# Kernel optimization log

Measured on AMD Instinct MI355X. Metric: run time of the kernel, lower is better.

Reference implementation:

```python
import jax, jax.numpy as jnp
import numpy as np

BIT = 8
QMAX = 2 ** (BIT - 1) - 1          # 127
QMIN = -(2 ** (BIT - 1))           # -128
BOUNDARY_RANGE = 0.005
EPS = 1e-5


def _quant_act_int8(x):
    # StatsQ per-tensor activation quantization: scale from (1 - boundary_range)
    # quantile of |x| (robust absmax), fake-quant with STE.
    amax = jnp.maximum(jnp.quantile(jnp.abs(x), 1.0 - BOUNDARY_RANGE), EPS)
    s = QMAX / amax
    q = jnp.clip(jnp.round(x * s), QMIN, QMAX) / s
    return x + jax.lax.stop_gradient(q - x)


def _quant_w_ternary(w):
    # BitNet-1.58-style per-tensor ternary weight quantization:
    # gamma = mean(|W|); W_q in {-1, 0, +1} * gamma; STE.
    gamma = jnp.mean(jnp.abs(w)) + EPS
    q = jnp.clip(jnp.round(w / gamma), -1.0, 1.0) * gamma
    return w + jax.lax.stop_gradient(q - w)


def _qlinear(x, w):
    # quantize activations (int8 fake-quant) and weights (ternary), then matmul
    xq = _quant_act_int8(x)
    wq = _quant_w_ternary(w)
    return jnp.einsum('btd,hd->bth', xq, wq)


def _layernorm(x, g, b):
    mu = jnp.mean(x, axis=-1, keepdims=True)
    var = jnp.mean(jnp.square(x - mu), axis=-1, keepdims=True)
    return (x - mu) * jax.lax.rsqrt(var + 1e-5) * g + b


def setup_inputs() -> dict:
    key = jax.random.key(0)
    k_x, k_w1, k_w2 = jax.random.split(key, 3)
    B, T, D, H = 64, 256, 1024, 4096
    x = jax.random.normal(k_x, (B, T, D), dtype=jnp.float32)
    ln_g = jnp.ones((D,), dtype=jnp.float32)
    ln_b = jnp.zeros((D,), dtype=jnp.float32)
    w1 = jax.random.normal(k_w1, (H, D), dtype=jnp.float32) * (1.0 / np.sqrt(D))
    w2 = jax.random.normal(k_w2, (D, H), dtype=jnp.float32) * (1.0 / np.sqrt(H))
    return {'x': x, 'ln_g': ln_g, 'ln_b': ln_b, 'w1': w1, 'w2': w2}


def reference(x, ln_g, ln_b, w1, w2):
    h = _layernorm(x, ln_g, ln_b)          # [B,T,D]
    h = _qlinear(h, w1)                    # [B,T,H]
    h = jax.nn.gelu(h, approximate=False)  # torch nn.GELU default = exact erf
    out = _qlinear(h, w2)                  # [B,T,D]
    return out
```

## Files before the change

kernel.cpp:

```cpp
#include <hip/hip_runtime.h>
#include <hip/hip_fp16.h>
#include <math.h>


#define M_ROWS 16384
#define D_DIM  1024
#define H_DIM  4096

typedef int i32x4 __attribute__((ext_vector_type(4)));

#define AS1 __attribute__((address_space(1)))
#define AS3 __attribute__((address_space(3)))

__device__ __forceinline__ void load_lds16(const void* g, void* l) {
  __builtin_amdgcn_global_load_lds((const AS1 void*)g, (AS3 void*)l, 16, 0, 0);
}

__device__ __forceinline__ float block_sum256(float v, float* lds) {
#pragma unroll
  for (int o = 32; o > 0; o >>= 1) v += __shfl_down(v, o, 64);
  int t = threadIdx.x;
  __syncthreads();
  if ((t & 63) == 0) lds[t >> 6] = v;
  __syncthreads();
  return lds[0] + lds[1] + lds[2] + lds[3];
}

__global__ __launch_bounds__(256) void k_layernorm(
    const float* __restrict__ x, const float* __restrict__ g,
    const float* __restrict__ b, __half* __restrict__ out) {
  __shared__ float lds[4];
  int row = blockIdx.x, t = threadIdx.x;
  float4 v = ((const float4*)(x + (size_t)row * D_DIM))[t];
  float s = v.x + v.y + v.z + v.w;
  s = block_sum256(s, lds);
  float mu = s * (1.0f / D_DIM);
  float d0 = v.x - mu, d1 = v.y - mu, d2 = v.z - mu, d3 = v.w - mu;
  float ss = d0 * d0 + d1 * d1 + d2 * d2 + d3 * d3;
  ss = block_sum256(ss, lds);
  float inv = 1.0f / sqrtf(ss * (1.0f / D_DIM) + 1e-5f);
  float4 gg = ((const float4*)g)[t];
  float4 bb = ((const float4*)b)[t];
  __half2 p0 = __floats2half2_rn(d0 * inv * gg.x + bb.x, d1 * inv * gg.y + bb.y);
  __half2 p1 = __floats2half2_rn(d2 * inv * gg.z + bb.z, d3 * inv * gg.w + bb.w);
  uint2 st;
  st.x = *(unsigned*)&p0;
  st.y = *(unsigned*)&p1;
  ((uint2*)(out + (size_t)row * D_DIM))[t] = st;
}

__global__ __launch_bounds__(256) void k_absmean(const float4* __restrict__ p,
                                                 size_t n4, double* __restrict__ out) {
  double s = 0.0;
  size_t stride = (size_t)gridDim.x * blockDim.x;
  for (size_t i = (size_t)blockIdx.x * blockDim.x + threadIdx.x; i < n4; i += stride) {
    float4 v = p[i];
    s += (double)fabsf(v.x) + (double)fabsf(v.y) + (double)fabsf(v.z) + (double)fabsf(v.w);
  }
#pragma unroll
  for (int o = 32; o > 0; o >>= 1) s += __shfl_down(s, o, 64);
  __shared__ double ds[4];
  int t = threadIdx.x;
  if ((t & 63) == 0) ds[t >> 6] = s;
  __syncthreads();
  if (t == 0) atomicAdd(out, ds[0] + ds[1] + ds[2] + ds[3]);
}

__device__ __forceinline__ int tern1(float w, float gamma) {
  return (int)fminf(1.f, fmaxf(-1.f, rintf(w / gamma)));
}

__global__ __launch_bounds__(256) void k_wquant(const float4* __restrict__ w,
                                                unsigned* __restrict__ wq, size_t n4,
                                                const double* __restrict__ sump,
                                                double inv_n, float* __restrict__ gamma_out) {
  float gamma = (float)(*sump * inv_n) + 1e-5f;
  if (blockIdx.x == 0 && threadIdx.x == 0) *gamma_out = gamma;
  size_t stride = (size_t)gridDim.x * blockDim.x;
  for (size_t i = (size_t)blockIdx.x * blockDim.x + threadIdx.x; i < n4; i += stride) {
    float4 v = w[i];
    int a = tern1(v.x, gamma), b = tern1(v.y, gamma), c = tern1(v.z, gamma), d = tern1(v.w, gamma);
    wq[i] = (unsigned)(a & 255) | ((unsigned)(b & 255) << 8) |
            ((unsigned)(c & 255) << 16) | ((unsigned)(d & 255) << 24);
  }
}

__global__ __launch_bounds__(512) void k_hist16(const uint4* __restrict__ p, size_t n8,
                                                unsigned* __restrict__ hist) {
  extern __shared__ unsigned h[];
  int t = threadIdx.x;
  for (int i = t; i < 32768; i += 512) h[i] = 0;
  __syncthreads();
  size_t stride = (size_t)gridDim.x * 512;
  for (size_t i = (size_t)blockIdx.x * 512 + t; i < n8; i += stride) {
    uint4 u = p[i];
    atomicAdd(&h[u.x & 0x7FFFu], 1u);
    atomicAdd(&h[(u.x >> 16) & 0x7FFFu], 1u);
    atomicAdd(&h[u.y & 0x7FFFu], 1u);
    atomicAdd(&h[(u.y >> 16) & 0x7FFFu], 1u);
    atomicAdd(&h[u.z & 0x7FFFu], 1u);
    atomicAdd(&h[(u.z >> 16) & 0x7FFFu], 1u);
    atomicAdd(&h[u.w & 0x7FFFu], 1u);
    atomicAdd(&h[(u.w >> 16) & 0x7FFFu], 1u);
  }
  __syncthreads();
  for (int i = t; i < 32768; i += 512) {
    unsigned c = h[i];
    if (c) atomicAdd(&hist[i], c);
  }
}

__global__ __launch_bounds__(256) void k_scanq(const unsigned* __restrict__ hist,
                                               float* __restrict__ scl,
                                               unsigned long long k, double frac) {
  __shared__ unsigned tsum[256];
  __shared__ unsigned long long pre[256];
  __shared__ unsigned vk, vk1;
  int t = threadIdx.x;
  unsigned s = 0;
  for (int j = 0; j < 128; ++j) s += hist[t * 128 + j];
  tsum[t] = s;
  __syncthreads();
  if (t == 0) {
    unsigned long long c = 0;
    for (int i = 0; i < 256; ++i) { pre[i] = c; c += tsum[i]; }
  }
  __syncthreads();
  unsigned long long base = pre[t];
  for (int j = 0; j < 128; ++j) {
    unsigned c = hist[t * 128 + j];
    if (base <= k && k < base + c) vk = t * 128 + j;
    if (base <= k + 1 && k + 1 < base + c) vk1 = t * 128 + j;
    base += c;
  }
  __syncthreads();
  if (t == 0) {
    double a = (double)__half2float(__ushort_as_half((unsigned short)vk));
    double b = (double)__half2float(__ushort_as_half((unsigned short)vk1));
    double qv = (frac >= 0.5) ? (b - (b - a) * (1.0 - frac)) : (a + (b - a) * frac);
    float amax = fmaxf((float)qv, 1e-5f);
    scl[0] = amax;
    scl[1] = 127.0f / amax;
  }
}

__device__ __forceinline__ void unpack8(uint4 u, float* f) {
  __half2 h;
  h = *(__half2*)&u.x; f[0] = __low2float(h); f[1] = __high2float(h);
  h = *(__half2*)&u.y; f[2] = __low2float(h); f[3] = __high2float(h);
  h = *(__half2*)&u.z; f[4] = __low2float(h); f[5] = __high2float(h);
  h = *(__half2*)&u.w; f[6] = __low2float(h); f[7] = __high2float(h);
}

__device__ __forceinline__ unsigned qpack4(float a, float b, float c, float d, float s) {
  int qa = (int)fminf(127.f, fmaxf(-128.f, rintf(a * s)));
  int qb = (int)fminf(127.f, fmaxf(-128.f, rintf(b * s)));
  int qc = (int)fminf(127.f, fmaxf(-128.f, rintf(c * s)));
  int qd = (int)fminf(127.f, fmaxf(-128.f, rintf(d * s)));
  return (unsigned)(qa & 255) | ((unsigned)(qb & 255) << 8) |
         ((unsigned)(qc & 255) << 16) | ((unsigned)(qd & 255) << 24);
}

__global__ __launch_bounds__(256) void k_quant16(const uint4* __restrict__ p,
                                                 uint2* __restrict__ q, size_t n8,
                                                 const float* __restrict__ scl) {
  float s = scl[1];
  size_t stride = (size_t)gridDim.x * blockDim.x;
  for (size_t i = (size_t)blockIdx.x * blockDim.x + threadIdx.x; i < n8; i += stride) {
    float f[8];
    unpack8(p[i], f);
    uint2 r;
    r.x = qpack4(f[0], f[1], f[2], f[3], s);
    r.y = qpack4(f[4], f[5], f[6], f[7], s);
    q[i] = r;
  }
}

__device__ __forceinline__ float gelu_fast(float v) {
  float a = fabsf(v) * 0.70710678118654752f;
  float t = __builtin_amdgcn_rcpf(fmaf(0.3275911f, a, 1.0f));
  float p = t * fmaf(t, fmaf(t, fmaf(t, fmaf(t, 1.061405429f, -1.453152027f),
                                     1.421413741f), -0.284496736f), 0.254829592f);
  float e = __expf(-a * a);
  float er = fmaf(-p, e, 1.0f);
  float erf_s = copysignf(er, v);
  return 0.5f * v * (1.0f + erf_s);
}

template <bool GELU>
__global__ __launch_bounds__(256) void k_gemm(const signed char* __restrict__ A,
                                              const signed char* __restrict__ B,
                                              int K, int N, void* __restrict__ outp,
                                              const float* __restrict__ gamma_p,
                                              const float* __restrict__ scl) {
  __shared__ __align__(16) signed char As[16384];
  __shared__ __align__(16) signed char Bs[16384];
  const int t = threadIdx.x;
  const int l = t & 63;
  const int wv = t >> 6;
  const int wr = (wv >> 1) * 64, wc = (wv & 1) * 64;
  const int m0 = blockIdx.y * 128, n0 = blockIdx.x * 128;

  const signed char* ag[4]; const signed char* bg[4];
  signed char* al[4]; signed char* bl[4];
#pragma unroll
  for (int c = 0; c < 4; ++c) {
    int g = c * 256 + t;
    int r = g >> 3;
    int cg = (g & 7) ^ (r & 7);
    ag[c] = A + (size_t)(m0 + r) * K + cg * 16;
    bg[c] = B + (size_t)(n0 + r) * K + cg * 16;
    al[c] = As + g * 16;
    bl[c] = Bs + g * 16;
  }

  int a_off[2][4], b_off[2][4];
#pragma unroll
  for (int s = 0; s < 2; ++s)
#pragma unroll
    for (int i = 0; i < 4; ++i) {
      int c = s * 4 + (l >> 4);
      int am = wr + i * 16 + (l & 15);
      a_off[s][i] = (am * 8 + (c ^ (am & 7))) * 16;
      int bn = wc + i * 16 + (l & 15);
      b_off[s][i] = (bn * 8 + (c ^ (bn & 7))) * 16;
    }

  i32x4 acc[4][4];
#pragma unroll
  for (int mi = 0; mi < 4; ++mi)
#pragma unroll
    for (int ni = 0; ni < 4; ++ni) {
      i32x4 z = {0, 0, 0, 0};
      acc[mi][ni] = z;
    }

  for (int kk = 0; kk < K; kk += 128) {
    __syncthreads();
#pragma unroll
    for (int c = 0; c < 4; ++c) {
      load_lds16(ag[c] + kk, al[c]);
      load_lds16(bg[c] + kk, bl[c]);
    }
    __syncthreads();
#pragma unroll
    for (int s = 0; s < 2; ++s) {
      i32x4 af[4], bf[4];
#pragma unroll
      for (int i = 0; i < 4; ++i) af[i] = *(const i32x4*)(As + a_off[s][i]);
#pragma unroll
      for (int i = 0; i < 4; ++i) bf[i] = *(const i32x4*)(Bs + b_off[s][i]);
#pragma unroll
      for (int mi = 0; mi < 4; ++mi)
#pragma unroll
        for (int ni = 0; ni < 4; ++ni)
          acc[mi][ni] = __builtin_amdgcn_mfma_i32_16x16x64_i8(af[mi], bf[ni], acc[mi][ni], 0, 0, 0);
    }
  }

  const float cs = (*gamma_p) / scl[1];
  const int col0 = n0 + wc + (l & 15);
  const int row00 = m0 + wr + (l >> 4) * 4;
#pragma unroll
  for (int mi = 0; mi < 4; ++mi) {
#pragma unroll
    for (int ni = 0; ni < 4; ++ni) {
      int col = col0 + ni * 16;
      int rbase = row00 + mi * 16;
#pragma unroll
      for (int r = 0; r < 4; ++r) {
        float v = cs * (float)acc[mi][ni][r];
        size_t idx = (size_t)(rbase + r) * N + col;
        if (GELU) {
          ((__half*)outp)[idx] = __float2half(gelu_fast(v));
        } else {
          ((float*)outp)[idx] = v;
        }
      }
    }
  }
}

extern "C" void kernel_launch(void* const* d_in, const int* in_sizes, int n_in,
                              void* d_out, int out_size, void* d_ws, size_t ws_size,
                              hipStream_t stream) {
  const float* x = (const float*)d_in[0];
  const float* ln_g = (const float*)d_in[1];
  const float* ln_b = (const float*)d_in[2];
  const float* w1 = (const float*)d_in[3];
  const float* w2 = (const float*)d_in[4];
  float* out = (float*)d_out;

  char* ws = (char*)d_ws;
  __half* h2 = (__half*)ws;
  __half* h1 = (__half*)(ws + ((size_t)128 << 20));
  signed char* xq1 = (signed char*)(ws + ((size_t)160 << 20));
  signed char* xq2 = (signed char*)(ws + ((size_t)128 << 20));
  signed char* w1q = (signed char*)(ws + ((size_t)192 << 20));
  signed char* w2q = (signed char*)(ws + ((size_t)196 << 20));
  char* sm = ws + ((size_t)200 << 20);
  unsigned* hista = (unsigned*)sm;
  unsigned* histb = (unsigned*)(sm + (128 << 10));
  double* wsum = (double*)(sm + (256 << 10));
  float* gamma = (float*)(sm + (256 << 10) + 16);
  float* scl1 = (float*)(sm + (256 << 10) + 32);
  float* scl2 = (float*)(sm + (256 << 10) + 40);

  hipMemsetAsync(sm, 0, (256 << 10) + 64, stream);

  hipFuncSetAttribute((const void*)k_hist16, hipFuncAttributeMaxDynamicSharedMemorySize,
                      131072);

  const double qq = 1.0 - 0.005;
  const unsigned long long N1 = (unsigned long long)M_ROWS * D_DIM;
  const unsigned long long N2 = (unsigned long long)M_ROWS * H_DIM;
  double idx1 = qq * (double)(N1 - 1);
  double idx2 = qq * (double)(N2 - 1);
  unsigned long long k1 = (unsigned long long)idx1;
  unsigned long long k2 = (unsigned long long)idx2;
  double frac1 = idx1 - (double)k1;
  double frac2 = idx2 - (double)k2;

  const size_t nW4 = (size_t)H_DIM * D_DIM / 4;
  const double inv_nW = 1.0 / (double)(H_DIM * D_DIM);

  k_absmean<<<512, 256, 0, stream>>>((const float4*)w1, nW4, wsum + 0);
  k_absmean<<<512, 256, 0, stream>>>((const float4*)w2, nW4, wsum + 1);
  k_wquant<<<1024, 256, 0, stream>>>((const float4*)w1, (unsigned*)w1q, nW4, wsum + 0, inv_nW, gamma + 0);
  k_wquant<<<1024, 256, 0, stream>>>((const float4*)w2, (unsigned*)w2q, nW4, wsum + 1, inv_nW, gamma + 1);

  k_layernorm<<<M_ROWS, 256, 0, stream>>>(x, ln_g, ln_b, h1);

  const size_t n8_1 = N1 / 8;
  k_hist16<<<256, 512, 131072, stream>>>((const uint4*)h1, n8_1, hista);
  k_scanq<<<1, 256, 0, stream>>>(hista, scl1, k1, frac1);
  k_quant16<<<1024, 256, 0, stream>>>((const uint4*)h1, (uint2*)xq1, n8_1, scl1);

  k_gemm<true><<<dim3(H_DIM / 128, M_ROWS / 128), 256, 0, stream>>>(
      xq1, w1q, D_DIM, H_DIM, (void*)h2, gamma + 0, scl1);

  const size_t n8_2 = N2 / 8;
  k_hist16<<<256, 512, 131072, stream>>>((const uint4*)h2, n8_2, histb);
  k_scanq<<<1, 256, 0, stream>>>(histb, scl2, k2, frac2);
  k_quant16<<<2048, 256, 0, stream>>>((const uint4*)h2, (uint2*)xq2, n8_2, scl2);

  k_gemm<false><<<dim3(D_DIM / 128, M_ROWS / 128), 256, 0, stream>>>(
      xq2, w2q, H_DIM, D_DIM, (void*)out, gamma + 1, scl2);
}
```

Before: 507.8 us.

## Switch int8 GEMM to 32x32x32 MFMA and merge weight-prep kernels

The int8 GEMM now uses mfma_i32_32x32x32_i8 with a 2x2 tile of 32x32 accumulators per wave instead of a 4x4 tile of 16x16x64 ops. The LDS fragment offsets and epilogue indexing are remapped to the new layout. K becomes a template parameter, the k-loop is partially unrolled by four, and launch_bounds now requests 4 blocks per CU. Separately, the two absmean and two weight-quantize launches are each merged into one kernel that splits its grid between w1 and w2, cutting launch count. The larger MFMA may change issue efficiency and register pressure.

```diff
diff --git a/kernel.cpp b/kernel.cpp
--- a/kernel.cpp
+++ b/kernel.cpp
@@ -8,6 +8,7 @@
 #define H_DIM  4096
 
 typedef int i32x4 __attribute__((ext_vector_type(4)));
+typedef int i32x16 __attribute__((ext_vector_type(16)));
 
 #define AS1 __attribute__((address_space(1)))
 #define AS3 __attribute__((address_space(3)))
@@ -49,11 +50,16 @@
   ((uint2*)(out + (size_t)row * D_DIM))[t] = st;
 }
 
-__global__ __launch_bounds__(256) void k_absmean(const float4* __restrict__ p,
-                                                 size_t n4, double* __restrict__ out) {
+__global__ __launch_bounds__(256) void k_absmean2(const float4* __restrict__ w1,
+                                                  const float4* __restrict__ w2,
+                                                  size_t n4, double* __restrict__ out) {
+  int which = (blockIdx.x >= (gridDim.x >> 1)) ? 1 : 0;
+  const float4* p = which ? w2 : w1;
+  unsigned half_grid = gridDim.x >> 1;
+  unsigned blk = blockIdx.x - which * half_grid;
   double s = 0.0;
-  size_t stride = (size_t)gridDim.x * blockDim.x;
-  for (size_t i = (size_t)blockIdx.x * blockDim.x + threadIdx.x; i < n4; i += stride) {
+  size_t stride = (size_t)half_grid * blockDim.x;
+  for (size_t i = (size_t)blk * blockDim.x + threadIdx.x; i < n4; i += stride) {
     float4 v = p[i];
     s += (double)fabsf(v.x) + (double)fabsf(v.y) + (double)fabsf(v.z) + (double)fabsf(v.w);
   }
@@ -63,21 +69,28 @@
   int t = threadIdx.x;
   if ((t & 63) == 0) ds[t >> 6] = s;
   __syncthreads();
-  if (t == 0) atomicAdd(out, ds[0] + ds[1] + ds[2] + ds[3]);
+  if (t == 0) atomicAdd(out + which, ds[0] + ds[1] + ds[2] + ds[3]);
 }
 
 __device__ __forceinline__ int tern1(float w, float gamma) {
   return (int)fminf(1.f, fmaxf(-1.f, rintf(w / gamma)));
 }
 
-__global__ __launch_bounds__(256) void k_wquant(const float4* __restrict__ w,
-                                                unsigned* __restrict__ wq, size_t n4,
-                                                const double* __restrict__ sump,
-                                                double inv_n, float* __restrict__ gamma_out) {
-  float gamma = (float)(*sump * inv_n) + 1e-5f;
-  if (blockIdx.x == 0 && threadIdx.x == 0) *gamma_out = gamma;
-  size_t stride = (size_t)gridDim.x * blockDim.x;
-  for (size_t i = (size_t)blockIdx.x * blockDim.x + threadIdx.x; i < n4; i += stride) {
+__global__ __launch_bounds__(256) void k_wquant2(const float4* __restrict__ w1,
+                                                 const float4* __restrict__ w2,
+                                                 unsigned* __restrict__ q1,
+                                                 unsigned* __restrict__ q2, size_t n4,
+                                                 const double* __restrict__ sump,
+                                                 double inv_n, float* __restrict__ gamma_out) {
+  int which = (blockIdx.x >= (gridDim.x >> 1)) ? 1 : 0;
+  const float4* w = which ? w2 : w1;
+  unsigned* wq = which ? q2 : q1;
+  unsigned half_grid = gridDim.x >> 1;
+  unsigned blk = blockIdx.x - which * half_grid;
+  float gamma = (float)(sump[which] * inv_n) + 1e-5f;
+  if (blk == 0 && threadIdx.x == 0) gamma_out[which] = gamma;
+  size_t stride = (size_t)half_grid * blockDim.x;
+  for (size_t i = (size_t)blk * blockDim.x + threadIdx.x; i < n4; i += stride) {
     float4 v = w[i];
     int a = tern1(v.x, gamma), b = tern1(v.y, gamma), c = tern1(v.z, gamma), d = tern1(v.w, gamma);
     wq[i] = (unsigned)(a & 255) | ((unsigned)(b & 255) << 8) |
@@ -187,12 +200,12 @@
   return 0.5f * v * (1.0f + erf_s);
 }
 
-template <bool GELU>
-__global__ __launch_bounds__(256) void k_gemm(const signed char* __restrict__ A,
-                                              const signed char* __restrict__ B,
-                                              int K, int N, void* __restrict__ outp,
-                                              const float* __restrict__ gamma_p,
-                                              const float* __restrict__ scl) {
+template <int K, bool GELU>
+__global__ __launch_bounds__(256, 4) void k_gemm(const signed char* __restrict__ A,
+                                                 const signed char* __restrict__ B,
+                                                 int N, void* __restrict__ outp,
+                                                 const float* __restrict__ gamma_p,
+                                                 const float* __restrict__ scl) {
   __shared__ __align__(16) signed char As[16384];
   __shared__ __align__(16) signed char Bs[16384];
   const int t = threadIdx.x;
@@ -216,61 +229,63 @@
 
   int a_off[2][4], b_off[2][4];
 #pragma unroll
-  for (int s = 0; s < 2; ++s)
-#pragma unroll
-    for (int i = 0; i < 4; ++i) {
-      int c = s * 4 + (l >> 4);
-      int am = wr + i * 16 + (l & 15);
-      a_off[s][i] = (am * 8 + (c ^ (am & 7))) * 16;
-      int bn = wc + i * 16 + (l & 15);
-      b_off[s][i] = (bn * 8 + (c ^ (bn & 7))) * 16;
+  for (int mi = 0; mi < 2; ++mi)
+#pragma unroll
+    for (int ks = 0; ks < 4; ++ks) {
+      int am = wr + mi * 32 + (l & 31);
+      int g = 2 * ks + (l >> 5);
+      a_off[mi][ks] = am * 128 + (g ^ (am & 7)) * 16;
+      int bn = wc + mi * 32 + (l & 31);
+      b_off[mi][ks] = bn * 128 + (g ^ (bn & 7)) * 16;
     }
 
-  i32x4 acc[4][4];
-#pragma unroll
-  for (int mi = 0; mi < 4; ++mi)
-#pragma unroll
-    for (int ni = 0; ni < 4; ++ni) {
-      i32x4 z = {0, 0, 0, 0};
-      acc[mi][ni] = z;
+  i32x16 acc[2][2];
+#pragma unroll
+  for (int mi = 0; mi < 2; ++mi)
+#pragma unroll
+    for (int ni = 0; ni < 2; ++ni)
+      acc[mi][ni] = (i32x16)(0);
+
+  for (int kk = 0; kk < K; kk += 512) {
+#pragma unroll
+    for (int j = 0; j < 4; ++j) {
+      const int ko = j * 128;
+      __syncthreads();
+#pragma unroll
+      for (int c = 0; c < 4; ++c) {
+        load_lds16(ag[c] + kk + ko, al[c]);
+        load_lds16(bg[c] + kk + ko, bl[c]);
+      }
+      __syncthreads();
+#pragma unroll
+      for (int ks = 0; ks < 4; ++ks) {
+        i32x4 af[2], bf[2];
+#pragma unroll
+        for (int i = 0; i < 2; ++i) af[i] = *(const i32x4*)(As + a_off[i][ks]);
+#pragma unroll
+        for (int i = 0; i < 2; ++i) bf[i] = *(const i32x4*)(Bs + b_off[i][ks]);
+#pragma unroll
+        for (int mi = 0; mi < 2; ++mi)
+#pragma unroll
+          for (int ni = 0; ni < 2; ++ni)
+            acc[mi][ni] = __builtin_amdgcn_mfma_i32_32x32x32_i8(af[mi], bf[ni], acc[mi][ni], 0, 0, 0);
+      }
     }
-
-  for (int kk = 0; kk < K; kk += 128) {
-    __syncthreads();
-#pragma unroll
-    for (int c = 0; c < 4; ++c) {
-      load_lds16(ag[c] + kk, al[c]);
-      load_lds16(bg[c] + kk, bl[c]);
-    }
-    __syncthreads();
-#pragma unroll
-    for (int s = 0; s < 2; ++s) {
-      i32x4 af[4], bf[4];
-#pragma unroll
-      for (int i = 0; i < 4; ++i) af[i] = *(const i32x4*)(As + a_off[s][i]);
-#pragma unroll
-      for (int i = 0; i < 4; ++i) bf[i] = *(const i32x4*)(Bs + b_off[s][i]);
-#pragma unroll
-      for (int mi = 0; mi < 4; ++mi)
-#pragma unroll
-        for (int ni = 0; ni < 4; ++ni)
-          acc[mi][ni] = __builtin_amdgcn_mfma_i32_16x16x64_i8(af[mi], bf[ni], acc[mi][ni], 0, 0, 0);
-    }
   }
 
   const float cs = (*gamma_p) / scl[1];
-  const int col0 = n0 + wc + (l & 15);
-  const int row00 = m0 + wr + (l >> 4) * 4;
-#pragma unroll
-  for (int mi = 0; mi < 4; ++mi) {
-#pragma unroll
-    for (int ni = 0; ni < 4; ++ni) {
-      int col = col0 + ni * 16;
-      int rbase = row00 + mi * 16;
-#pragma unroll
-      for (int r = 0; r < 4; ++r) {
-        float v = cs * (float)acc[mi][ni][r];
-        size_t idx = (size_t)(rbase + r) * N + col;
+  const int col0 = n0 + wc + (l & 31);
+  const int row0 = m0 + wr + 4 * (l >> 5);
+#pragma unroll
+  for (int mi = 0; mi < 2; ++mi) {
+#pragma unroll
+    for (int ni = 0; ni < 2; ++ni) {
+      int col = col0 + ni * 32;
+#pragma unroll
+      for (int reg = 0; reg < 16; ++reg) {
+        int row = row0 + mi * 32 + (reg & 3) + 8 * (reg >> 2);
+        float v = cs * (float)acc[mi][ni][reg];
+        size_t idx = (size_t)row * N + col;
         if (GELU) {
           ((__half*)outp)[idx] = __float2half(gelu_fast(v));
         } else {
@@ -307,7 +322,6 @@
   float* scl2 = (float*)(sm + (256 << 10) + 40);
 
   hipMemsetAsync(sm, 0, (256 << 10) + 64, stream);
-
   hipFuncSetAttribute((const void*)k_hist16, hipFuncAttributeMaxDynamicSharedMemorySize,
                       131072);
 
@@ -324,10 +338,9 @@
   const size_t nW4 = (size_t)H_DIM * D_DIM / 4;
   const double inv_nW = 1.0 / (double)(H_DIM * D_DIM);
 
-  k_absmean<<<512, 256, 0, stream>>>((const float4*)w1, nW4, wsum + 0);
-  k_absmean<<<512, 256, 0, stream>>>((const float4*)w2, nW4, wsum + 1);
-  k_wquant<<<1024, 256, 0, stream>>>((const float4*)w1, (unsigned*)w1q, nW4, wsum + 0, inv_nW, gamma + 0);
-  k_wquant<<<1024, 256, 0, stream>>>((const float4*)w2, (unsigned*)w2q, nW4, wsum + 1, inv_nW, gamma + 1);
+  k_absmean2<<<1024, 256, 0, stream>>>((const float4*)w1, (const float4*)w2, nW4, wsum);
+  k_wquant2<<<2048, 256, 0, stream>>>((const float4*)w1, (const float4*)w2,
+                                      (unsigned*)w1q, (unsigned*)w2q, nW4, wsum, inv_nW, gamma);
 
   k_layernorm<<<M_ROWS, 256, 0, stream>>>(x, ln_g, ln_b, h1);
 
@@ -336,14 +349,14 @@
   k_scanq<<<1, 256, 0, stream>>>(hista, scl1, k1, frac1);
   k_quant16<<<1024, 256, 0, stream>>>((const uint4*)h1, (uint2*)xq1, n8_1, scl1);
 
-  k_gemm<true><<<dim3(H_DIM / 128, M_ROWS / 128), 256, 0, stream>>>(
-      xq1, w1q, D_DIM, H_DIM, (void*)h2, gamma + 0, scl1);
+  k_gemm<D_DIM, true><<<dim3(H_DIM / 128, M_ROWS / 128), 256, 0, stream>>>(
+      xq1, w1q, H_DIM, (void*)h2, gamma + 0, scl1);
 
   const size_t n8_2 = N2 / 8;
   k_hist16<<<256, 512, 131072, stream>>>((const uint4*)h2, n8_2, histb);
   k_scanq<<<1, 256, 0, stream>>>(histb, scl2, k2, frac2);
   k_quant16<<<2048, 256, 0, stream>>>((const uint4*)h2, (uint2*)xq2, n8_2, scl2);
 
-  k_gemm<false><<<dim3(D_DIM / 128, M_ROWS / 128), 256, 0, stream>>>(
-      xq2, w2q, H_DIM, D_DIM, (void*)out, gamma + 1, scl2);
-}
+  k_gemm<H_DIM, false><<<dim3(D_DIM / 128, M_ROWS / 128), 256, 0, stream>>>(
+      xq2, w2q, D_DIM, (void*)out, gamma + 1, scl2);
+}
```

New measurement: 479.8 us. 5.5% less time.
